# Kernel optimization log

Hardware: AMD Instinct MI355X
Metric: run time of the kernel (lower is better)

## Reference

```python
import jax, jax.numpy as jnp
import numpy as np


def setup_inputs() -> dict:
    key = jax.random.key(0)
    k1, k2, k3 = jax.random.split(key, 3)
    n, c, h, w = 32, 384, 56, 56
    m, d_model = 8, 768
    x = jax.random.normal(k1, (n, c, h, w), dtype=jnp.float32)
    global_feature = jax.random.normal(k2, (n, m, d_model), dtype=jnp.float32)
    # Linear(d_model, 2*c): torch weight shape (2c, d_model)
    W_kv = jax.random.normal(k3, (2 * c, d_model), dtype=jnp.float32) * (1.0 / np.sqrt(d_model))
    b_kv = jnp.zeros((2 * c,), dtype=jnp.float32)
    return {"x": x, "global_feature": global_feature, "W_kv": W_kv, "b_kv": b_kv}


def reference(x, global_feature, W_kv, b_kv):
    n, c, h, w = x.shape
    # MLP (single Linear + ReLU6, no BN since bn=False)
    kv = jnp.einsum('nmd,ed->nme', global_feature, W_kv) + b_kv  # [n, m, 2c]
    kv = jnp.clip(kv, 0.0, 6.0)  # ReLU6
    K = kv[:, :, :c]   # [n, m, c]
    V = kv[:, :, c:]   # [n, m, c]
    q = x.reshape(n, c, h * w).transpose(0, 2, 1)  # [n, hw, c]
    scores = jnp.einsum('nqc,nkc->nqk', q, K)       # [n, hw, m] (unscaled)
    attn = jax.nn.softmax(scores, axis=-1)
    v_agg = jnp.einsum('nqk,nkc->nqc', attn, V)     # [n, hw, c]
    feature = v_agg.transpose(0, 2, 1).reshape(n, c, h, w)
    return feature + x
```

## Files before the change

kernel.cpp:

```cpp
#include <hip/hip_runtime.h>


#define NC 384
#define HWP 3136
#define DD 768
#define MM 8
#define EE 768

__global__ __launch_bounds__(256) void kv_kernel(const float* __restrict__ gf,
                                                 const float* __restrict__ Wk,
                                                 const float* __restrict__ bk,
                                                 float* __restrict__ kv) {
    __shared__ float g[MM * DD];
    const int n = blockIdx.y;
    const int et = blockIdx.x;
    const int t = threadIdx.x;

    const float* gfn = gf + (size_t)n * (MM * DD);
    for (int i = t; i < MM * DD; i += 256) g[i] = gfn[i];
    __syncthreads();

    const int e = et * 64 + (t & 63);
    const int mb = (t >> 6) * 2;

    const float4* w4 = (const float4*)(Wk + (size_t)e * DD);
    const float4* g0 = (const float4*)(g + (mb + 0) * DD);
    const float4* g1 = (const float4*)(g + (mb + 1) * DD);

    float a0 = 0.f, a1 = 0.f;
    #pragma unroll 8
    for (int i = 0; i < DD / 4; ++i) {
        const float4 w = w4[i];
        const float4 v0 = g0[i];
        const float4 v1 = g1[i];
        a0 += w.x * v0.x + w.y * v0.y + w.z * v0.z + w.w * v0.w;
        a1 += w.x * v1.x + w.y * v1.y + w.z * v1.z + w.w * v1.w;
    }
    const float bv = bk[e];
    float* o = kv + (size_t)n * (MM * EE);
    o[(mb + 0) * EE + e] = fminf(fmaxf(a0 + bv, 0.f), 6.f);
    o[(mb + 1) * EE + e] = fminf(fmaxf(a1 + bv, 0.f), 6.f);
}

__global__ __launch_bounds__(256, 4) void attn_kernel(const float* __restrict__ x,
                                                      const float* __restrict__ kv,
                                                      float* __restrict__ out) {
    __shared__ float kvs[6144];
    __shared__ float sc[4][8][32];

    const int n = blockIdx.y;
    const int tile = blockIdx.x;
    const int t = threadIdx.x;
    const int p2 = t & 15;
    const int gq = t >> 4;
    const int w = t >> 6;
    const int c0 = gq * 24;
    const int pos0 = tile * 32 + p2 * 2;

    const float4* kvn4 = (const float4*)(kv + (size_t)n * (MM * EE));
    float4* kvs4 = (float4*)kvs;
    #pragma unroll
    for (int r = 0; r < 6; ++r) {
        const int f = t + r * 256;
        const int k = f / 192;
        const int e4 = f - k * 192;
        const int half = (e4 >= 96) ? 1 : 0;
        const int c4 = e4 - half * 96;
        kvs4[half * 768 + k * 96 + c4] = kvn4[f];
    }
    __syncthreads();
    __builtin_amdgcn_sched_barrier(0);

    const float* xp = x + (size_t)n * NC * HWP + (size_t)c0 * HWP + pos0;
    float2 xr[24];
    #pragma unroll
    for (int i = 0; i < 24; ++i) xr[i] = *(const float2*)(xp + (size_t)i * HWP);

    float accx[8], accy[8];
    #pragma unroll
    for (int k = 0; k < 8; ++k) { accx[k] = 0.f; accy[k] = 0.f; }

    const float* kbase = &kvs[gq * 24];
    #pragma unroll
    for (int i4 = 0; i4 < 6; ++i4) {
        const float2 x0 = xr[i4 * 4 + 0];
        const float2 x1 = xr[i4 * 4 + 1];
        const float2 x2 = xr[i4 * 4 + 2];
        const float2 x3 = xr[i4 * 4 + 3];
        #pragma unroll
        for (int k = 0; k < 8; ++k) {
            const float4 kk = *(const float4*)&kbase[k * 384 + i4 * 4];
            accx[k] += x0.x * kk.x + x1.x * kk.y + x2.x * kk.z + x3.x * kk.w;
            accy[k] += x0.y * kk.x + x1.y * kk.y + x2.y * kk.z + x3.y * kk.w;
        }
    }

    #pragma unroll
    for (int k = 0; k < 8; ++k) {
        accx[k] += __shfl_xor(accx[k], 16, 64);
        accx[k] += __shfl_xor(accx[k], 32, 64);
        accy[k] += __shfl_xor(accy[k], 16, 64);
        accy[k] += __shfl_xor(accy[k], 32, 64);
    }
    if ((t & 48) == 0) {
        #pragma unroll
        for (int k = 0; k < 8; ++k)
            *(float2*)&sc[w][k][p2 * 2] = make_float2(accx[k], accy[k]);
    }
    __syncthreads();

    float sx[8], sy[8];
    #pragma unroll
    for (int k = 0; k < 8; ++k) {
        float2 s = *(const float2*)&sc[0][k][p2 * 2];
        #pragma unroll
        for (int ww = 1; ww < 4; ++ww) {
            const float2 q = *(const float2*)&sc[ww][k][p2 * 2];
            s.x += q.x; s.y += q.y;
        }
        sx[k] = s.x; sy[k] = s.y;
    }
    {
        float mx = sx[0], my = sy[0];
        #pragma unroll
        for (int k = 1; k < 8; ++k) { mx = fmaxf(mx, sx[k]); my = fmaxf(my, sy[k]); }
        float sux = 0.f, suy = 0.f;
        #pragma unroll
        for (int k = 0; k < 8; ++k) {
            sx[k] = __expf(sx[k] - mx); sux += sx[k];
            sy[k] = __expf(sy[k] - my); suy += sy[k];
        }
        const float ix = 1.f / sux, iy = 1.f / suy;
        #pragma unroll
        for (int k = 0; k < 8; ++k) { sx[k] *= ix; sy[k] *= iy; }
    }

    float* op = out + (size_t)n * NC * HWP + (size_t)c0 * HWP + pos0;
    const float* vbase = &kvs[3072 + gq * 24];
    #pragma unroll
    for (int i4 = 0; i4 < 6; ++i4) {
        float2 o0 = xr[i4 * 4 + 0];
        float2 o1 = xr[i4 * 4 + 1];
        float2 o2 = xr[i4 * 4 + 2];
        float2 o3 = xr[i4 * 4 + 3];
        #pragma unroll
        for (int k = 0; k < 8; ++k) {
            const float4 vv = *(const float4*)&vbase[k * 384 + i4 * 4];
            o0.x += sx[k] * vv.x; o0.y += sy[k] * vv.x;
            o1.x += sx[k] * vv.y; o1.y += sy[k] * vv.y;
            o2.x += sx[k] * vv.z; o2.y += sy[k] * vv.z;
            o3.x += sx[k] * vv.w; o3.y += sy[k] * vv.w;
        }
        *(float2*)(op + (size_t)(i4 * 4 + 0) * HWP) = o0;
        *(float2*)(op + (size_t)(i4 * 4 + 1) * HWP) = o1;
        *(float2*)(op + (size_t)(i4 * 4 + 2) * HWP) = o2;
        *(float2*)(op + (size_t)(i4 * 4 + 3) * HWP) = o3;
    }
}

extern "C" void kernel_launch(void* const* d_in, const int* in_sizes, int n_in,
                              void* d_out, int out_size, void* d_ws, size_t ws_size,
                              hipStream_t stream) {
    const float* x  = (const float*)d_in[0];
    const float* gf = (const float*)d_in[1];
    const float* Wk = (const float*)d_in[2];
    const float* bk = (const float*)d_in[3];
    float* out = (float*)d_out;
    float* kv = (float*)d_ws;

    kv_kernel<<<dim3(12, 32), 256, 0, stream>>>(gf, Wk, bk, kv);
    attn_kernel<<<dim3(98, 32), 256, 0, stream>>>(x, kv, out);
}
```

Before: 317.8 us.

## Restructure kv projection to coalesced register-held weight rows with lane reductions

The kv_kernel now has each 16-lane group own one output feature. The group holds that feature's weight row in registers using coalesced float4 loads and reduces the dot products across lanes with shuffles. Each block handles two batch items, so weights are reused across them, and the grid grows to 48x16 blocks. This is meant to replace the strided per-thread weight-row reads of the old layout and to raise parallelism in the small projection kernel. The cost is extra shuffle reductions and a second shared-memory reload.

Result: faster. 287.9 us (-9.4%).

```diff
diff --git a/kernel.cpp b/kernel.cpp
--- a/kernel.cpp
+++ b/kernel.cpp
@@ -12,34 +12,50 @@
                                                  const float* __restrict__ bk,
                                                  float* __restrict__ kv) {
     __shared__ float g[MM * DD];
-    const int n = blockIdx.y;
-    const int et = blockIdx.x;
     const int t = threadIdx.x;
+    const int lane = t & 63;
+    const int w = t >> 6;
+    const int grp = lane >> 4;
+    const int lq = lane & 15;
+    const int e = blockIdx.x * 16 + w * 4 + grp;
 
-    const float* gfn = gf + (size_t)n * (MM * DD);
-    for (int i = t; i < MM * DD; i += 256) g[i] = gfn[i];
-    __syncthreads();
+    float4 wr[12];
+    const float* wrow = Wk + (size_t)e * DD;
+    #pragma unroll
+    for (int j = 0; j < 12; ++j)
+        wr[j] = *(const float4*)(wrow + j * 64 + lq * 4);
+    const float bv = bk[e];
 
-    const int e = et * 64 + (t & 63);
-    const int mb = (t >> 6) * 2;
+    #pragma unroll
+    for (int ni = 0; ni < 2; ++ni) {
+        const int n = blockIdx.y * 2 + ni;
+        if (ni) __syncthreads();
+        const float4* gfn = (const float4*)(gf + (size_t)n * (MM * DD));
+        float4* g4 = (float4*)g;
+        #pragma unroll
+        for (int r = 0; r < 6; ++r) g4[t + r * 256] = gfn[t + r * 256];
+        __syncthreads();
 
-    const float4* w4 = (const float4*)(Wk + (size_t)e * DD);
-    const float4* g0 = (const float4*)(g + (mb + 0) * DD);
-    const float4* g1 = (const float4*)(g + (mb + 1) * DD);
-
-    float a0 = 0.f, a1 = 0.f;
-    #pragma unroll 8
-    for (int i = 0; i < DD / 4; ++i) {
-        const float4 w = w4[i];
-        const float4 v0 = g0[i];
-        const float4 v1 = g1[i];
-        a0 += w.x * v0.x + w.y * v0.y + w.z * v0.z + w.w * v0.w;
-        a1 += w.x * v1.x + w.y * v1.y + w.z * v1.z + w.w * v1.w;
+        float res = 0.f;
+        #pragma unroll
+        for (int m = 0; m < 8; ++m) {
+            float acc = 0.f;
+            #pragma unroll
+            for (int j = 0; j < 12; ++j) {
+                const float4 gg = *(const float4*)&g[m * DD + j * 64 + lq * 4];
+                acc += wr[j].x * gg.x + wr[j].y * gg.y
+                     + wr[j].z * gg.z + wr[j].w * gg.w;
+            }
+            acc += __shfl_xor(acc, 1, 64);
+            acc += __shfl_xor(acc, 2, 64);
+            acc += __shfl_xor(acc, 4, 64);
+            acc += __shfl_xor(acc, 8, 64);
+            if (lq == m) res = acc;
+        }
+        if (lq < 8)
+            kv[(size_t)n * (MM * EE) + (size_t)lq * EE + e] =
+                fminf(fmaxf(res + bv, 0.f), 6.f);
     }
-    const float bv = bk[e];
-    float* o = kv + (size_t)n * (MM * EE);
-    o[(mb + 0) * EE + e] = fminf(fmaxf(a0 + bv, 0.f), 6.f);
-    o[(mb + 1) * EE + e] = fminf(fmaxf(a1 + bv, 0.f), 6.f);
 }
 
 __global__ __launch_bounds__(256, 4) void attn_kernel(const float* __restrict__ x,
@@ -168,6 +184,6 @@
     float* out = (float*)d_out;
     float* kv = (float*)d_ws;
 
-    kv_kernel<<<dim3(12, 32), 256, 0, stream>>>(gf, Wk, bk, kv);
+    kv_kernel<<<dim3(48, 16), 256, 0, stream>>>(gf, Wk, bk, kv);
     attn_kernel<<<dim3(98, 32), 256, 0, stream>>>(x, kv, out);
 }
```
